# Performance work log

Hardware: AMD Instinct MI355X
Metric: run time of the kernel (lower is better)

The kernel has to match this reference:

```python
import jax, jax.numpy as jnp
import numpy as np

N, T = 64, 256
V, E, K = 32000, 256, 128


def setup_inputs() -> dict:
    key = jax.random.key(0)
    ks = jax.random.split(key, 7)
    x = jax.random.randint(ks[0], (N, T), 0, V)
    embed_w = jax.random.normal(ks[1], (V, E), dtype=jnp.float32) * 0.02
    # nn.Linear(embed_dim, K*K, bias=False), weight.uniform_(-1, 1)
    trans_w = jax.random.uniform(ks[2], (K * K, E), dtype=jnp.float32, minval=-1.0, maxval=1.0)
    # nn.Linear(1, K): weight [K,1], bias [K]
    start_w = jax.random.normal(ks[3], (K, 1), dtype=jnp.float32)
    start_b = jax.random.normal(ks[4], (K,), dtype=jnp.float32) * 0.1
    # nn.Embedding(K, K) cluster embeddings
    emb_cluster_w = jax.random.normal(ks[5], (K, K), dtype=jnp.float32)
    # nn.Linear(K, vocab, bias=False), weight.uniform_(-1, 1) -> weight [V, K]
    emit_w = jax.random.uniform(ks[6], (V, K), dtype=jnp.float32, minval=-1.0, maxval=1.0)
    return {"x": x, "embed_w": embed_w, "trans_w": trans_w, "start_w": start_w,
            "start_b": start_b, "emb_cluster_w": emb_cluster_w, "emit_w": emit_w}


def reference(x, embed_w, trans_w, start_w, start_b, emb_cluster_w, emit_w):
    n, t = x.shape
    k = emb_cluster_w.shape[0]
    ex = embed_w[x]                                            # [N,T,E]
    # Emissions: log_softmax(emit(emb_cluster(i))) per cluster -> [K,V]
    log_emit = jax.nn.log_softmax(emb_cluster_w @ emit_w.T, axis=-1)
    log_emit_t = log_emit.T                                    # [V,K]
    # start(dummy): ones[N,1] @ W.T + b = W[:,0]+b, same per row
    pre = jax.nn.log_softmax(start_w[:, 0] + start_b)          # [K]
    pre = jnp.broadcast_to(pre, (n, k))
    xs = (jnp.swapaxes(ex[:, :-1, :], 0, 1),                   # [T-1,N,E]
          x[:, 1:].T)                                          # [T-1,N]
    def step(pre_alpha, inp):
        x_prev, w_t = inp
        tran = jax.nn.log_softmax((x_prev @ trans_w.T).reshape(n, k, k), axis=-1)
        cur = jax.nn.logsumexp(pre_alpha[:, :, None] + tran, axis=1)   # [N,K]
        cur = cur + log_emit_t[w_t]                            # add log p(w_t | state)
        return cur, None
    cur, _ = jax.lax.scan(step, pre, xs)
    return -jnp.mean(jax.nn.logsumexp(cur, axis=1))
```

## Files before the change

kernel.cpp:

```cpp
#include <hip/hip_runtime.h>
#include <cstdint>
#include <cstddef>

#define N_SEQ 64
#define T_LEN 256
#define VOCAB 32000
#define EDIM  256
#define KS    128
#define KK    16384
#define MROWS 16384
#define MREAL 16320
#define GPART 16

typedef short  short8  __attribute__((ext_vector_type(8)));
typedef float  floatx4 __attribute__((ext_vector_type(4)));
typedef int    intx8   __attribute__((ext_vector_type(8)));

#define LGKM_BARRIER() asm volatile("s_waitcnt lgkmcnt(0)\n\ts_barrier" ::: "memory")
#define LGKM_WAIT()    asm volatile("s_waitcnt lgkmcnt(0)" ::: "memory")

static __device__ __forceinline__ unsigned short f2bf(float f) {
  unsigned u = __float_as_uint(f);
  u += 0x7fffu + ((u >> 16) & 1u);
  return (unsigned short)(u >> 16);
}

static __device__ __forceinline__ float fast_rcp(float x) {
#if __has_builtin(__builtin_amdgcn_rcpf)
  return __builtin_amdgcn_rcpf(x);
#else
  return 1.0f / x;
#endif
}

static __device__ __forceinline__ void gl_lds16(const void* gptr, void* lptr) {
  __builtin_amdgcn_global_load_lds(
      (const __attribute__((address_space(1))) void*)gptr,
      (__attribute__((address_space(3))) void*)lptr, 16, 0, 0);
}

__global__ __launch_bounds__(128) void k_prep(const float* sw, const float* sb, float* pre0) {
  __shared__ float vals[KS];
  __shared__ float MM, LS;
  int tid = threadIdx.x;
  float v = sw[tid] + sb[tid];
  vals[tid] = v;
  __syncthreads();
  if (tid == 0) { float m = vals[0]; for (int i = 1; i < KS; ++i) m = fmaxf(m, vals[i]); MM = m; }
  __syncthreads();
  float e = __expf(v - MM);
  vals[tid] = e;
  __syncthreads();
  if (tid == 0) { float s = 0.f; for (int i = 0; i < KS; ++i) s += vals[i]; LS = MM + __logf(s); }
  __syncthreads();
  pre0[tid] = v - LS;
}

__global__ __launch_bounds__(256) void k_transcvt(const float* tw, unsigned short* tb) {
  int idx = blockIdx.x * 256 + threadIdx.x;
  if (idx >= (KK * EDIM) / 4) return;
  int row = idx >> 6, e4 = idx & 63;
  int rowp = ((row & 127) << 7) | (row >> 7);
  int e4s = (e4 & 0x31) | (((((e4 >> 1) & 7) ^ (rowp & 7))) << 1);
  float4 v = *(const float4*)&tw[(size_t)idx * 4];
  unsigned h0 = f2bf(v.x), h1 = f2bf(v.y), h2 = f2bf(v.z), h3 = f2bf(v.w);
  uint2 o; o.x = h0 | (h1 << 16); o.y = h2 | (h3 << 16);
  *(uint2*)&tb[(size_t)rowp * EDIM + e4s * 4] = o;
}

__global__ __launch_bounds__(256) void k_embed(const int* x, const float* ew, unsigned short* exb) {
  int m = blockIdx.x, e = threadIdx.x;
  int t = m >> 6, n = m & 63;
  float v = 0.f;
  if (m < MREAL) { int tok = x[n * T_LEN + t]; v = ew[(size_t)tok * EDIM + e]; }
  int es = (e & 0xC7) | ((((e >> 3) & 7) ^ (m & 7)) << 3);
  exb[(size_t)m * EDIM + es] = f2bf(v);
}

__global__ __launch_bounds__(256) void k_emitlogits(const float* ecl, const float* emw, float* C) {
  int v0 = blockIdx.x * 64, k0 = blockIdx.y * 64;
  int tid = threadIdx.x;
  __shared__ alignas(16) float At[64 * 17];
  __shared__ alignas(16) float Bt[64 * 17];
  int tx = tid & 15, ty = tid >> 4;
  int r = tid >> 2, q = tid & 3;
  float acc[4][4] = {};
  for (int d0 = 0; d0 < KS; d0 += 16) {
    float4 av = *(const float4*)&ecl[(size_t)(k0 + r) * KS + d0 + q * 4];
    float4 bv = *(const float4*)&emw[(size_t)(v0 + r) * KS + d0 + q * 4];
    __syncthreads();
    At[r * 17 + q * 4 + 0] = av.x; At[r * 17 + q * 4 + 1] = av.y;
    At[r * 17 + q * 4 + 2] = av.z; At[r * 17 + q * 4 + 3] = av.w;
    Bt[r * 17 + q * 4 + 0] = bv.x; Bt[r * 17 + q * 4 + 1] = bv.y;
    Bt[r * 17 + q * 4 + 2] = bv.z; Bt[r * 17 + q * 4 + 3] = bv.w;
    __syncthreads();
    #pragma unroll
    for (int dd = 0; dd < 16; ++dd) {
      float a[4], b[4];
      #pragma unroll
      for (int i = 0; i < 4; ++i) a[i] = At[(ty * 4 + i) * 17 + dd];
      #pragma unroll
      for (int i = 0; i < 4; ++i) b[i] = Bt[(tx * 4 + i) * 17 + dd];
      #pragma unroll
      for (int i = 0; i < 4; ++i)
        #pragma unroll
        for (int jj = 0; jj < 4; ++jj) acc[i][jj] += a[i] * b[jj];
    }
  }
  #pragma unroll
  for (int i = 0; i < 4; ++i) {
    float4 o; o.x = acc[i][0]; o.y = acc[i][1]; o.z = acc[i][2]; o.w = acc[i][3];
    *(float4*)&C[(size_t)(k0 + ty * 4 + i) * VOCAB + v0 + tx * 4] = o;
  }
}

__global__ __launch_bounds__(256) void k_lsec(const float* C, float* lseC) {
  int k = blockIdx.x, tid = threadIdx.x;
  __shared__ float sm[4], ss[4];
  const float* row = C + (size_t)k * VOCAB;
  float m = -1e30f;
  for (int v = tid; v < VOCAB; v += 256) m = fmaxf(m, row[v]);
  #pragma unroll
  for (int s = 1; s < 64; s <<= 1) m = fmaxf(m, __shfl_xor(m, s));
  if ((tid & 63) == 0) sm[tid >> 6] = m;
  __syncthreads();
  m = fmaxf(fmaxf(sm[0], sm[1]), fmaxf(sm[2], sm[3]));
  float sum = 0.f;
  for (int v = tid; v < VOCAB; v += 256) sum += __expf(row[v] - m);
  #pragma unroll
  for (int s = 1; s < 64; s <<= 1) sum += __shfl_xor(sum, s);
  if ((tid & 63) == 0) ss[tid >> 6] = sum;
  __syncthreads();
  if (tid == 0) lseC[k] = m + __logf(ss[0] + ss[1] + ss[2] + ss[3]);
}

__global__ __launch_bounds__(128) void k_emis(const int* x, const float* C, const float* lseC,
                                              float* emis, float* emax) {
  int t = blockIdx.x + 1;
  int n = blockIdx.y;
  int k = threadIdx.x;
  __shared__ float red[2];
  int w = x[n * T_LEN + t];
  float v = C[(size_t)k * VOCAB + w] - lseC[k];
  emis[(size_t)((n << 8) + t) * KS + k] = v;
  float m = v;
  #pragma unroll
  for (int s = 1; s < 64; s <<= 1) m = fmaxf(m, __shfl_xor(m, s));
  if ((k & 63) == 0) red[k >> 6] = m;
  __syncthreads();
  if (k == 0) emax[n * T_LEN + t] = fmaxf(red[0], red[1]);
}

__global__ __launch_bounds__(256) void k_comb(const float* srowP, float* srowR, float* wcomb,
                                              const float* emis, const float* emax,
                                              int m_base, int Rcap, int rows) {
  int id = blockIdx.x * 256 + threadIdx.x;
  if (id >= rows * KS) return;
  float s = 0.f;
  #pragma unroll
  for (int g = 0; g < GPART; ++g) s += srowP[(size_t)g * Rcap * KS + id];
  float r = 1.0f / s;
  srowR[(size_t)m_base * KS + id] = r;
  int m = m_base + (id >> 7);
  int t = m >> 6, n = m & 63, k = id & 127;
  float wv = 0.f;
  if (t >= 1) {
    float e  = emis[(size_t)((n << 8) + t) * KS + k];
    float ex = emax[n * T_LEN + t];
    wv = __expf(e - ex) * r * 4096.0f;
  }
  wcomb[(size_t)m_base * KS + id] = wv;
}

static __device__ __forceinline__ void scan_load_S(const unsigned char* Sbase,
                                                   int l15, int kg, intx8 (&sf)[8]) {
  #pragma unroll
  for (int q = 0; q < 8; ++q) {
    const uint4* p = (const uint4*)(Sbase + (size_t)(q * 16 + l15) * 128 + kg * 32);
    uint4 a = p[0], b = p[1];
    sf[q][0] = a.x; sf[q][1] = a.y; sf[q][2] = a.z; sf[q][3] = a.w;
    sf[q][4] = b.x; sf[q][5] = b.y; sf[q][6] = b.z; sf[q][7] = b.w;
  }
}

static __device__ __forceinline__ void scan_step2(
    int t, int t0, int tLast, int n, int l15, int kg,
    const unsigned char* Sc, const float* wcomb, const float* emax,
    unsigned char* uL8, intx8 (&sf)[8], intx8& uf,
    float (&wv)[8], float& exR, float& M) {
  const float LNS = 8.317766167f;
  floatx4 cz = {0.f, 0.f, 0.f, 0.f};
  float cv[8];
  #pragma unroll
  for (int q = 0; q < 8; ++q) {
    floatx4 d = __builtin_amdgcn_mfma_scale_f32_16x16x128_f8f6f4(
        uf, sf[q], cz, 0, 0, 0, 0x7F7F7F7F, 0, 0x7F7F7F7F);
    cv[q] = d[0];
  }
  int tp = t + 2; if (tp > tLast) tp = tLast;
  scan_load_S(Sc + (size_t)((tp - t0) * 64 + n) * KK, l15, kg, sf);
  float c0 = __uint_as_float(__builtin_amdgcn_readfirstlane(__float_as_uint(cv[0])));
  float rc = fast_rcp(c0);
  #pragma unroll
  for (int q = 0; q < 8; ++q) {
    float up = cv[q] * wv[q] * rc;
    int pk = __builtin_amdgcn_cvt_pk_fp8_f32(up, up, 0, 0);
    uL8[q * 16 + l15] = (unsigned char)(pk & 0xff);
  }
  M += exR + __logf(c0) - LNS;
  #pragma unroll
  for (int q = 0; q < 8; ++q) wv[q] = wcomb[(size_t)(tp * 64 + n) * KS + q * 16 + l15];
  exR = emax[n * T_LEN + tp];
  LGKM_WAIT();
  {
    uint4 ua = *(const uint4*)&uL8[kg * 32];
    uint4 ub = *(const uint4*)&uL8[kg * 32 + 16];
    uf[0] = ua.x; uf[1] = ua.y; uf[2] = ua.z; uf[3] = ua.w;
    uf[4] = ub.x; uf[5] = ub.y; uf[6] = ub.z; uf[7] = ub.w;
  }
}

__global__ __launch_bounds__(256, 2) void k_fused(
    const unsigned short* exb, const unsigned short* trb,
    unsigned char* Sg, float* srowP, int m_base, int Rcap,
    const unsigned char* Ss, const float* srowR, const float* wcomb,
    const float* emis, const float* emax, const float* pre0,
    float* alphaG, float* nll, int t0s, int tcs) {
  __shared__ alignas(16) unsigned short As[128 * 64];
  __shared__ alignas(16) unsigned short Bs[128 * 64];
  __shared__ alignas(16) unsigned char uL8[KS];

  if (blockIdx.x < 64) {
    if (tcs <= 0 || threadIdx.x >= 64) return;
    int n = blockIdx.x;
    int L = threadIdx.x, l15 = L & 15, kg = L >> 4;
    const float SCALE = 4096.0f;
    const float LNS = 8.317766167f;
    int t1 = t0s + tcs, tLast = t1 - 1;
    const float* a0 = (t0s == 1) ? pre0 : (alphaG + (size_t)n * KS);
    float pre[8];
    #pragma unroll
    for (int q = 0; q < 8; ++q) pre[q] = a0[q * 16 + l15];
    float mx = pre[0];
    #pragma unroll
    for (int q = 1; q < 8; ++q) mx = fmaxf(mx, pre[q]);
    #pragma unroll
    for (int s2 = 1; s2 < 16; s2 <<= 1) mx = fmaxf(mx, __shfl_xor(mx, s2));
    float M = mx;
    #pragma unroll
    for (int q = 0; q < 8; ++q) {
      float r0 = srowR[(size_t)((t0s - 1) * 64 + n) * KS + q * 16 + l15];
      float up = __expf(pre[q] - M) * r0 * SCALE;
      int pk = __builtin_amdgcn_cvt_pk_fp8_f32(up, up, 0, 0);
      uL8[q * 16 + l15] = (unsigned char)(pk & 0xff);
    }
    LGKM_WAIT();
    intx8 uf;
    {
      uint4 ua = *(const uint4*)&uL8[kg * 32];
      uint4 ub = *(const uint4*)&uL8[kg * 32 + 16];
      uf[0] = ua.x; uf[1] = ua.y; uf[2] = ua.z; uf[3] = ua.w;
      uf[4] = ub.x; uf[5] = ub.y; uf[6] = ub.z; uf[7] = ub.w;
    }
    intx8 sfA[8], sfB[8];
    scan_load_S(Ss + (size_t)n * KK, l15, kg, sfA);
    int tB = (t0s + 1 < t1) ? (t0s + 1) : tLast;
    scan_load_S(Ss + (size_t)((tB - t0s) * 64 + n) * KK, l15, kg, sfB);
    float wA[8], wB[8];
    #pragma unroll
    for (int q = 0; q < 8; ++q) {
      wA[q] = wcomb[(size_t)(t0s * 64 + n) * KS + q * 16 + l15];
      wB[q] = wcomb[(size_t)(tB * 64 + n) * KS + q * 16 + l15];
    }
    float exA = emax[n * T_LEN + t0s];
    float exB = emax[n * T_LEN + tB];
    int t = t0s;
    while (t < tLast) {
      scan_step2(t, t0s, tLast, n, l15, kg, Ss, wcomb, emax, uL8, sfA, uf, wA, exA, M);
      ++t;
      if (t >= tLast) break;
      scan_step2(t, t0s, tLast, n, l15, kg, Ss, wcomb, emax, uL8, sfB, uf, wB, exB, M);
      ++t;
    }
    {
      floatx4 cz = {0.f, 0.f, 0.f, 0.f};
      float cv[8];
      #pragma unroll
      for (int q = 0; q < 8; ++q) {
        floatx4 d = __builtin_amdgcn_mfma_scale_f32_16x16x128_f8f6f4(
            uf, sfA[q], cz, 0, 0, 0, 0x7F7F7F7F, 0, 0x7F7F7F7F);
        cv[q] = d[0];
      }
      #pragma unroll
      for (int q = 0; q < 8; ++q) {
        float em = emis[(size_t)((n << 8) + tLast) * KS + q * 16 + l15];
        pre[q] = M - LNS + __logf(cv[q]) + em;
      }
    }
    #pragma unroll
    for (int q = 0; q < 8; ++q) alphaG[(size_t)n * KS + q * 16 + l15] = pre[q];
    if (t1 == T_LEN) {
      float m2 = pre[0];
      #pragma unroll
      for (int q = 1; q < 8; ++q) m2 = fmaxf(m2, pre[q]);
      #pragma unroll
      for (int s2 = 1; s2 < 16; s2 <<= 1) m2 = fmaxf(m2, __shfl_xor(m2, s2));
      float e = 0.f;
      #pragma unroll
      for (int q = 0; q < 8; ++q) e += __expf(pre[q] - m2);
      #pragma unroll
      for (int s2 = 1; s2 < 16; s2 <<= 1) e += __shfl_xor(e, s2);
      if (L == 0) nll[n] = m2 + __logf(e);
    }
    return;
  }

  int g = blockIdx.x - 64;
  int bx = g >> 4, grp = g & 15;
  int tid = threadIdx.x, wv = tid >> 6, ln = tid & 63;
  int wc = wv & 1, wm = wv >> 1;
  int m0 = m_base + bx * 128;
  int lr = ln & 15, lk = (ln >> 4) * 8;
  int lg = ln >> 4;
  floatx4 sacc[4][4] = {};
  for (int byi = 0; byi < 8; ++byi) {
    int by = grp * 8 + byi;
    int c0 = by * 128;
    floatx4 acc[4][4] = {};
    for (int k0 = 0; k0 < EDIM; k0 += 64) {
      #pragma unroll
      for (int r = 0; r < 4; ++r) {
        int chunk = (wv * 4 + r) * 64 + ln;
        int row = chunk >> 3, c8 = chunk & 7;
        gl_lds16(&exb[(size_t)(m0 + row) * EDIM + k0 + c8 * 8], &As[(wv * 4 + r) * 512]);
        gl_lds16(&trb[(size_t)(c0 + row) * EDIM + k0 + c8 * 8], &Bs[(wv * 4 + r) * 512]);
      }
      __syncthreads();
      #pragma unroll
      for (int kk = 0; kk < 64; kk += 32) {
        int sw = ((((kk + lk) >> 3) ^ (lr & 7)) << 3);
        short8 af[4], bf[4];
        #pragma unroll
        for (int f = 0; f < 4; ++f)
          af[f] = *(const short8*)&As[(wm * 64 + f * 16 + lr) * 64 + sw];
        #pragma unroll
        for (int f = 0; f < 4; ++f)
          bf[f] = *(const short8*)&Bs[(wc * 64 + f * 16 + lr) * 64 + sw];
        #pragma unroll
        for (int fc = 0; fc < 4; ++fc)
          #pragma unroll
          for (int fm = 0; fm < 4; ++fm)
            acc[fc][fm] = __builtin_amdgcn_mfma_f32_16x16x32_bf16(bf[fc], af[fm], acc[fc][fm], 0, 0, 0);
      }
      LGKM_BARRIER();
    }
    unsigned char* Ts = (unsigned char*)As;
    #pragma unroll
    for (int fc = 0; fc < 4; ++fc) {
      #pragma unroll
      for (int fm = 0; fm < 4; ++fm) {
        floatx4 a = acc[fc][fm];
        float e0 = __expf(a[0]), e1 = __expf(a[1]), e2 = __expf(a[2]), e3 = __expf(a[3]);
        int p = __builtin_amdgcn_cvt_pk_fp8_f32(e0, e1, 0, 0);
        p = __builtin_amdgcn_cvt_pk_fp8_f32(e2, e3, p, 1);
        int mloc = wm * 64 + fm * 16 + lr;
        int cl = wc * 64 + fc * 16 + lg * 4;
        *(int*)&Ts[mloc * 128 + (cl ^ ((mloc & 7) << 4))] = p;
        sacc[fc][fm][0] += e0; sacc[fc][fm][1] += e1;
        sacc[fc][fm][2] += e2; sacc[fc][fm][3] += e3;
      }
    }
    LGKM_BARRIER();
    #pragma unroll
    for (int r = 0; r < 4; ++r) {
      int seg = r * 256 + tid;
      int mloc = seg >> 3, s = seg & 7;
      uint4 v = *(const uint4*)&Ts[mloc * 128 + ((s ^ (mloc & 7)) << 4)];
      *(uint4*)&Sg[(size_t)(bx * 128 + mloc) * KK + c0 + s * 16] = v;
    }
    LGKM_BARRIER();
  }
  #pragma unroll
  for (int fc = 0; fc < 4; ++fc) {
    #pragma unroll
    for (int fm = 0; fm < 4; ++fm) {
      int mloc = bx * 128 + wm * 64 + fm * 16 + lr;
      int i = wc * 64 + fc * 16 + lg * 4;
      *(floatx4*)&srowP[((size_t)grp * Rcap + mloc) * KS + i] = sacc[fc][fm];
    }
  }
}

__global__ __launch_bounds__(64) void k_final(const float* nll, float* out) {
  int tid = threadIdx.x;
  float v = nll[tid];
  #pragma unroll
  for (int s = 1; s < 64; s <<= 1) v += __shfl_xor(v, s);
  if (tid == 0) out[0] = -v / 64.0f;
}

extern "C" void kernel_launch(void* const* d_in, const int* in_sizes, int n_in,
                              void* d_out, int out_size, void* d_ws, size_t ws_size,
                              hipStream_t stream) {
  const int*   x       = (const int*)d_in[0];
  const float* embed_w = (const float*)d_in[1];
  const float* trans_w = (const float*)d_in[2];
  const float* start_w = (const float*)d_in[3];
  const float* start_b = (const float*)d_in[4];
  const float* ecl     = (const float*)d_in[5];
  const float* emw     = (const float*)d_in[6];

  char* w = (char*)d_ws;
  size_t off = 0;
  auto alloc = [&](size_t bytes) -> char* {
    char* p = w + off;
    off = (off + bytes + 255) & ~(size_t)255;
    return p;
  };
  float*          pre0   = (float*)alloc(KS * 4);
  float*          lseC   = (float*)alloc(KS * 4);
  float*          nll    = (float*)alloc(N_SEQ * 4);
  float*          alphaG = (float*)alloc((size_t)N_SEQ * KS * 4);
  float*          emax   = (float*)alloc((size_t)N_SEQ * T_LEN * 4);
  unsigned short* trb    = (unsigned short*)alloc((size_t)KK * EDIM * 2);
  unsigned short* exb    = (unsigned short*)alloc((size_t)MROWS * EDIM * 2);
  float*          emis   = (float*)alloc((size_t)N_SEQ * T_LEN * KS * 4);
  float*          srowR  = (float*)alloc((size_t)MROWS * KS * 4);
  float*          wcomb  = (float*)alloc((size_t)MROWS * KS * 4);
  char* region = w + off;
  size_t avail = (ws_size > off) ? (ws_size - off) : 0;
  float* C = (float*)region;

  int Tc = 2;
  for (int c = 2; c <= 64; c += 2)
    if ((size_t)c * 64 * 40960 <= avail) Tc = c;
  int Rcap = Tc * 64;
  unsigned char* S0    = (unsigned char*)region;
  unsigned char* S1    = (unsigned char*)(region + (size_t)Rcap * KK);
  float*         srowP = (float*)(region + (size_t)2 * Rcap * KK);

  hipLaunchKernelGGL(k_prep,       dim3(1),        dim3(128), 0, stream, start_w, start_b, pre0);
  hipLaunchKernelGGL(k_transcvt,   dim3(4096),     dim3(256), 0, stream, trans_w, trb);
  hipLaunchKernelGGL(k_embed,      dim3(16384),    dim3(256), 0, stream, x, embed_w, exb);
  hipLaunchKernelGGL(k_emitlogits, dim3(500, 2),   dim3(256), 0, stream, ecl, emw, C);
  hipLaunchKernelGGL(k_lsec,       dim3(128),      dim3(256), 0, stream, C, lseC);
  hipLaunchKernelGGL(k_emis,       dim3(255, 64),  dim3(128), 0, stream, x, C, lseC, emis, emax);

  int ct0[140], ctc[140], nc = 0;
  {
    int t0 = 1;
    while (t0 < T_LEN) {
      int tc = T_LEN - t0; if (tc > Tc) tc = Tc;
      ct0[nc] = t0; ctc[nc] = tc; ++nc; t0 += tc;
    }
  }
  for (int c = 0; c <= nc; ++c) {
    bool hasG = (c < nc), hasS = (c > 0);
    int gx = 0, m_base = 0;
    if (hasG) { gx = (ctc[c] * 64 + 127) / 128; m_base = (ct0[c] - 1) * 64; }
    unsigned char* Sg = (c & 1) ? S1 : S0;
    unsigned char* Ssc = ((c - 1) & 1) ? S1 : S0;
    int t0s = hasS ? ct0[c - 1] : 0;
    int tcs = hasS ? ctc[c - 1] : 0;
    hipLaunchKernelGGL(k_fused, dim3(64 + gx * 16), dim3(256), 0, stream,
                       exb, trb, Sg, srowP, m_base, Rcap,
                       Ssc, srowR, wcomb, emis, emax, pre0, alphaG, nll, t0s, tcs);
    if (hasG)
      hipLaunchKernelGGL(k_comb, dim3(gx * 64), dim3(256), 0, stream,
                         srowP, srowR, wcomb, emis, emax, m_base, Rcap, gx * 128);
  }
  hipLaunchKernelGGL(k_final, dim3(1), dim3(64), 0, stream, nll, (float*)d_out);
}
```

Measured before the change: 576.3 us.

## Stage scan transition tiles into LDS with triple-buffered async global-to-LDS loads

The scan blocks now stream each step's fp8 transition tile and combined weights into a three-slot LDS ring using global_load_lds, prefetching two steps ahead and waiting with vmcnt, instead of holding two register copies of the tile. The weight buffer is transposed to an [n,t,k] layout so each step's weights form one contiguous 512-byte load. The per-step emax accumulation is replaced by a single wave reduction at the start, and the logs are summed and applied once at the end. This is meant to hide global latency on the serial recurrence and cut register pressure, at the cost of LDS reads per step and a shared-memory union with the GEMM path.

```diff
diff --git a/kernel.cpp b/kernel.cpp
--- a/kernel.cpp
+++ b/kernel.cpp
@@ -37,6 +37,16 @@
   __builtin_amdgcn_global_load_lds(
       (const __attribute__((address_space(1))) void*)gptr,
       (__attribute__((address_space(3))) void*)lptr, 16, 0, 0);
+}
+
+static __device__ __forceinline__ void stage_S(const unsigned char* src,
+                                               unsigned char* dst, int p) {
+  #pragma unroll
+  for (int j = 0; j < 16; ++j) {
+    int A = j * 1024 + p * 16;
+    int gg = A ^ (((A >> 7) & 7) << 4);
+    gl_lds16(src + gg, dst + j * 1024);
+  }
 }
 
 __global__ __launch_bounds__(128) void k_prep(const float* sw, const float* sb, float* pre0) {
@@ -151,7 +161,7 @@
   if (k == 0) emax[n * T_LEN + t] = fmaxf(red[0], red[1]);
 }
 
-__global__ __launch_bounds__(256) void k_comb(const float* srowP, float* srowR, float* wcomb,
+__global__ __launch_bounds__(256) void k_comb(const float* srowP, float* srowR, float* wcombT,
                                               const float* emis, const float* emax,
                                               int m_base, int Rcap, int rows) {
   int id = blockIdx.x * 256 + threadIdx.x;
@@ -169,73 +179,30 @@
     float ex = emax[n * T_LEN + t];
     wv = __expf(e - ex) * r * 4096.0f;
   }
-  wcomb[(size_t)m_base * KS + id] = wv;
-}
-
-static __device__ __forceinline__ void scan_load_S(const unsigned char* Sbase,
-                                                   int l15, int kg, intx8 (&sf)[8]) {
-  #pragma unroll
-  for (int q = 0; q < 8; ++q) {
-    const uint4* p = (const uint4*)(Sbase + (size_t)(q * 16 + l15) * 128 + kg * 32);
-    uint4 a = p[0], b = p[1];
-    sf[q][0] = a.x; sf[q][1] = a.y; sf[q][2] = a.z; sf[q][3] = a.w;
-    sf[q][4] = b.x; sf[q][5] = b.y; sf[q][6] = b.z; sf[q][7] = b.w;
-  }
-}
-
-static __device__ __forceinline__ void scan_step2(
-    int t, int t0, int tLast, int n, int l15, int kg,
-    const unsigned char* Sc, const float* wcomb, const float* emax,
-    unsigned char* uL8, intx8 (&sf)[8], intx8& uf,
-    float (&wv)[8], float& exR, float& M) {
-  const float LNS = 8.317766167f;
-  floatx4 cz = {0.f, 0.f, 0.f, 0.f};
-  float cv[8];
-  #pragma unroll
-  for (int q = 0; q < 8; ++q) {
-    floatx4 d = __builtin_amdgcn_mfma_scale_f32_16x16x128_f8f6f4(
-        uf, sf[q], cz, 0, 0, 0, 0x7F7F7F7F, 0, 0x7F7F7F7F);
-    cv[q] = d[0];
-  }
-  int tp = t + 2; if (tp > tLast) tp = tLast;
-  scan_load_S(Sc + (size_t)((tp - t0) * 64 + n) * KK, l15, kg, sf);
-  float c0 = __uint_as_float(__builtin_amdgcn_readfirstlane(__float_as_uint(cv[0])));
-  float rc = fast_rcp(c0);
-  #pragma unroll
-  for (int q = 0; q < 8; ++q) {
-    float up = cv[q] * wv[q] * rc;
-    int pk = __builtin_amdgcn_cvt_pk_fp8_f32(up, up, 0, 0);
-    uL8[q * 16 + l15] = (unsigned char)(pk & 0xff);
-  }
-  M += exR + __logf(c0) - LNS;
-  #pragma unroll
-  for (int q = 0; q < 8; ++q) wv[q] = wcomb[(size_t)(tp * 64 + n) * KS + q * 16 + l15];
-  exR = emax[n * T_LEN + tp];
-  LGKM_WAIT();
-  {
-    uint4 ua = *(const uint4*)&uL8[kg * 32];
-    uint4 ub = *(const uint4*)&uL8[kg * 32 + 16];
-    uf[0] = ua.x; uf[1] = ua.y; uf[2] = ua.z; uf[3] = ua.w;
-    uf[4] = ub.x; uf[5] = ub.y; uf[6] = ub.z; uf[7] = ub.w;
-  }
+  wcombT[((size_t)n * T_LEN + t) * KS + k] = wv;
 }
 
 __global__ __launch_bounds__(256, 2) void k_fused(
     const unsigned short* exb, const unsigned short* trb,
     unsigned char* Sg, float* srowP, int m_base, int Rcap,
-    const unsigned char* Ss, const float* srowR, const float* wcomb,
+    const unsigned char* Ss, const float* srowR, const float* wcombT,
     const float* emis, const float* emax, const float* pre0,
     float* alphaG, float* nll, int t0s, int tcs) {
-  __shared__ alignas(16) unsigned short As[128 * 64];
-  __shared__ alignas(16) unsigned short Bs[128 * 64];
+  __shared__ union alignas(16) {
+    struct { unsigned short As[128 * 64]; unsigned short Bs[128 * 64]; } g;
+    struct { unsigned char S3[3][16384]; unsigned char aux3[3][1024]; } s;
+  } sh;
   __shared__ alignas(16) unsigned char uL8[KS];
 
   if (blockIdx.x < 64) {
     if (tcs <= 0 || threadIdx.x >= 64) return;
     int n = blockIdx.x;
-    int L = threadIdx.x, l15 = L & 15, kg = L >> 4;
+    int p = threadIdx.x;
+    int l15 = p & 15, kg = p >> 4;
+    int swz = (l15 & 7) << 4;
     const float SCALE = 4096.0f;
     const float LNS = 8.317766167f;
+    int L = tcs;
     int t1 = t0s + tcs, tLast = t1 - 1;
     const float* a0 = (t0s == 1) ? pre0 : (alphaG + (size_t)n * KS);
     float pre[8];
@@ -247,6 +214,10 @@
     #pragma unroll
     for (int s2 = 1; s2 < 16; s2 <<= 1) mx = fmaxf(mx, __shfl_xor(mx, s2));
     float M = mx;
+    float ev = (p < L - 1) ? emax[n * T_LEN + t0s + p] : 0.f;
+    #pragma unroll
+    for (int s2 = 1; s2 < 64; s2 <<= 1) ev += __shfl_xor(ev, s2);
+    float exSum = ev;
     #pragma unroll
     for (int q = 0; q < 8; ++q) {
       float r0 = srowR[(size_t)((t0s - 1) * 64 + n) * KS + q * 16 + l15];
@@ -255,6 +226,7 @@
       uL8[q * 16 + l15] = (unsigned char)(pk & 0xff);
     }
     LGKM_WAIT();
+    __builtin_amdgcn_sched_barrier(0);
     intx8 uf;
     {
       uint4 ua = *(const uint4*)&uL8[kg * 32];
@@ -262,40 +234,63 @@
       uf[0] = ua.x; uf[1] = ua.y; uf[2] = ua.z; uf[3] = ua.w;
       uf[4] = ub.x; uf[5] = ub.y; uf[6] = ub.z; uf[7] = ub.w;
     }
-    intx8 sfA[8], sfB[8];
-    scan_load_S(Ss + (size_t)n * KK, l15, kg, sfA);
-    int tB = (t0s + 1 < t1) ? (t0s + 1) : tLast;
-    scan_load_S(Ss + (size_t)((tB - t0s) * 64 + n) * KK, l15, kg, sfB);
-    float wA[8], wB[8];
-    #pragma unroll
-    for (int q = 0; q < 8; ++q) {
-      wA[q] = wcomb[(size_t)(t0s * 64 + n) * KS + q * 16 + l15];
-      wB[q] = wcomb[(size_t)(tB * 64 + n) * KS + q * 16 + l15];
-    }
-    float exA = emax[n * T_LEN + t0s];
-    float exB = emax[n * T_LEN + tB];
-    int t = t0s;
-    while (t < tLast) {
-      scan_step2(t, t0s, tLast, n, l15, kg, Ss, wcomb, emax, uL8, sfA, uf, wA, exA, M);
-      ++t;
-      if (t >= tLast) break;
-      scan_step2(t, t0s, tLast, n, l15, kg, Ss, wcomb, emax, uL8, sfB, uf, wB, exB, M);
-      ++t;
-    }
-    {
+    const unsigned char* wcb = (const unsigned char*)wcombT;
+    stage_S(Ss + (size_t)n * KK, &sh.s.S3[0][0], p);
+    gl_lds16(wcb + ((size_t)n * T_LEN + t0s) * 512 + (size_t)p * 16, &sh.s.aux3[0][0]);
+    int i1 = (1 < L) ? 1 : (L - 1);
+    stage_S(Ss + (size_t)(i1 * 64 + n) * KK, &sh.s.S3[1][0], p);
+    gl_lds16(wcb + ((size_t)n * T_LEN + (t0s + i1)) * 512 + (size_t)p * 16, &sh.s.aux3[1][0]);
+
+    float logSum = 0.f;
+    int bu = 0, bs = 2;
+    for (int i = 0; i < L; ++i) {
+      int ip2 = i + 2; if (ip2 > L - 1) ip2 = L - 1;
+      stage_S(Ss + (size_t)(ip2 * 64 + n) * KK, &sh.s.S3[bs][0], p);
+      gl_lds16(wcb + ((size_t)n * T_LEN + (t0s + ip2)) * 512 + (size_t)p * 16, &sh.s.aux3[bs][0]);
+      asm volatile("s_waitcnt vmcnt(34)" ::: "memory");
+      __builtin_amdgcn_sched_barrier(0);
+      const unsigned char* Sb = &sh.s.S3[bu][0];
       floatx4 cz = {0.f, 0.f, 0.f, 0.f};
       float cv[8];
       #pragma unroll
       for (int q = 0; q < 8; ++q) {
+        int ab = (((q * 16 + l15) * 128) + kg * 32) ^ swz;
+        uint4 aa = *(const uint4*)&Sb[ab];
+        uint4 bb = *(const uint4*)&Sb[ab ^ 16];
+        intx8 sf;
+        sf[0] = aa.x; sf[1] = aa.y; sf[2] = aa.z; sf[3] = aa.w;
+        sf[4] = bb.x; sf[5] = bb.y; sf[6] = bb.z; sf[7] = bb.w;
         floatx4 d = __builtin_amdgcn_mfma_scale_f32_16x16x128_f8f6f4(
-            uf, sfA[q], cz, 0, 0, 0, 0x7F7F7F7F, 0, 0x7F7F7F7F);
+            uf, sf, cz, 0, 0, 0, 0x7F7F7F7F, 0, 0x7F7F7F7F);
         cv[q] = d[0];
       }
-      #pragma unroll
-      for (int q = 0; q < 8; ++q) {
-        float em = emis[(size_t)((n << 8) + tLast) * KS + q * 16 + l15];
-        pre[q] = M - LNS + __logf(cv[q]) + em;
+      if (i < L - 1) {
+        float c0 = __uint_as_float(__builtin_amdgcn_readfirstlane(__float_as_uint(cv[0])));
+        float rc = fast_rcp(c0);
+        const float* wvp = (const float*)&sh.s.aux3[bu][0];
+        #pragma unroll
+        for (int q = 0; q < 8; ++q) {
+          float up = cv[q] * wvp[q * 16 + l15] * rc;
+          int pk = __builtin_amdgcn_cvt_pk_fp8_f32(up, up, 0, 0);
+          uL8[q * 16 + l15] = (unsigned char)(pk & 0xff);
+        }
+        logSum += __logf(c0);
+        LGKM_WAIT();
+        __builtin_amdgcn_sched_barrier(0);
+        uint4 ua = *(const uint4*)&uL8[kg * 32];
+        uint4 ub = *(const uint4*)&uL8[kg * 32 + 16];
+        uf[0] = ua.x; uf[1] = ua.y; uf[2] = ua.z; uf[3] = ua.w;
+        uf[4] = ub.x; uf[5] = ub.y; uf[6] = ub.z; uf[7] = ub.w;
+      } else {
+        float Mf = M + exSum + logSum - (float)(L - 1) * LNS;
+        #pragma unroll
+        for (int q = 0; q < 8; ++q) {
+          float em = emis[(size_t)((n << 8) + tLast) * KS + q * 16 + l15];
+          pre[q] = Mf - LNS + __logf(cv[q]) + em;
+        }
       }
+      bu = (bu == 2) ? 0 : bu + 1;
+      bs = (bs == 2) ? 0 : bs + 1;
     }
     #pragma unroll
     for (int q = 0; q < 8; ++q) alphaG[(size_t)n * KS + q * 16 + l15] = pre[q];
@@ -310,7 +305,7 @@
       for (int q = 0; q < 8; ++q) e += __expf(pre[q] - m2);
       #pragma unroll
       for (int s2 = 1; s2 < 16; s2 <<= 1) e += __shfl_xor(e, s2);
-      if (L == 0) nll[n] = m2 + __logf(e);
+      if (p == 0) nll[n] = m2 + __logf(e);
     }
     return;
   }
@@ -332,8 +327,8 @@
       for (int r = 0; r < 4; ++r) {
         int chunk = (wv * 4 + r) * 64 + ln;
         int row = chunk >> 3, c8 = chunk & 7;
-        gl_lds16(&exb[(size_t)(m0 + row) * EDIM + k0 + c8 * 8], &As[(wv * 4 + r) * 512]);
-        gl_lds16(&trb[(size_t)(c0 + row) * EDIM + k0 + c8 * 8], &Bs[(wv * 4 + r) * 512]);
+        gl_lds16(&exb[(size_t)(m0 + row) * EDIM + k0 + c8 * 8], &sh.g.As[(wv * 4 + r) * 512]);
+        gl_lds16(&trb[(size_t)(c0 + row) * EDIM + k0 + c8 * 8], &sh.g.Bs[(wv * 4 + r) * 512]);
       }
       __syncthreads();
       #pragma unroll
@@ -342,10 +337,10 @@
         short8 af[4], bf[4];
         #pragma unroll
         for (int f = 0; f < 4; ++f)
-          af[f] = *(const short8*)&As[(wm * 64 + f * 16 + lr) * 64 + sw];
+          af[f] = *(const short8*)&sh.g.As[(wm * 64 + f * 16 + lr) * 64 + sw];
         #pragma unroll
         for (int f = 0; f < 4; ++f)
-          bf[f] = *(const short8*)&Bs[(wc * 64 + f * 16 + lr) * 64 + sw];
+          bf[f] = *(const short8*)&sh.g.Bs[(wc * 64 + f * 16 + lr) * 64 + sw];
         #pragma unroll
         for (int fc = 0; fc < 4; ++fc)
           #pragma unroll
@@ -354,18 +349,18 @@
       }
       LGKM_BARRIER();
     }
-    unsigned char* Ts = (unsigned char*)As;
+    unsigned char* Ts = (unsigned char*)sh.g.As;
     #pragma unroll
     for (int fc = 0; fc < 4; ++fc) {
       #pragma unroll
       for (int fm = 0; fm < 4; ++fm) {
         floatx4 a = acc[fc][fm];
         float e0 = __expf(a[0]), e1 = __expf(a[1]), e2 = __expf(a[2]), e3 = __expf(a[3]);
-        int p = __builtin_amdgcn_cvt_pk_fp8_f32(e0, e1, 0, 0);
-        p = __builtin_amdgcn_cvt_pk_fp8_f32(e2, e3, p, 1);
+        int pq = __builtin_amdgcn_cvt_pk_fp8_f32(e0, e1, 0, 0);
+        pq = __builtin_amdgcn_cvt_pk_fp8_f32(e2, e3, pq, 1);
         int mloc = wm * 64 + fm * 16 + lr;
         int cl = wc * 64 + fc * 16 + lg * 4;
-        *(int*)&Ts[mloc * 128 + (cl ^ ((mloc & 7) << 4))] = p;
+        *(int*)&Ts[mloc * 128 + (cl ^ ((mloc & 7) << 4))] = pq;
         sacc[fc][fm][0] += e0; sacc[fc][fm][1] += e1;
         sacc[fc][fm][2] += e2; sacc[fc][fm][3] += e3;
       }
@@ -426,7 +421,7 @@
   unsigned short* exb    = (unsigned short*)alloc((size_t)MROWS * EDIM * 2);
   float*          emis   = (float*)alloc((size_t)N_SEQ * T_LEN * KS * 4);
   float*          srowR  = (float*)alloc((size_t)MROWS * KS * 4);
-  float*          wcomb  = (float*)alloc((size_t)MROWS * KS * 4);
+  float*          wcombT = (float*)alloc((size_t)N_SEQ * T_LEN * KS * 4);
   char* region = w + off;
   size_t avail = (ws_size > off) ? (ws_size - off) : 0;
   float* C = (float*)region;
@@ -464,10 +459,10 @@
     int tcs = hasS ? ctc[c - 1] : 0;
     hipLaunchKernelGGL(k_fused, dim3(64 + gx * 16), dim3(256), 0, stream,
                        exb, trb, Sg, srowP, m_base, Rcap,
-                       Ssc, srowR, wcomb, emis, emax, pre0, alphaG, nll, t0s, tcs);
+                       Ssc, srowR, wcombT, emis, emax, pre0, alphaG, nll, t0s, tcs);
     if (hasG)
       hipLaunchKernelGGL(k_comb, dim3(gx * 64), dim3(256), 0, stream,
-                         srowP, srowR, wcomb, emis, emax, m_base, Rcap, gx * 128);
+                         srowP, srowR, wcombT, emis, emax, m_base, Rcap, gx * 128);
   }
   hipLaunchKernelGGL(k_final, dim3(1), dim3(64), 0, stream, nll, (float*)d_out);
 }
```

Result: slower. 612.3 us (+6.2%).

## Replace partial-sum buffers and combine kernel with atomic row-sum accumulation

Applied to the files above, without the earlier changes.

The GEMM blocks now atomically add their per-group row sums directly into a zeroed srowS buffer, instead of writing 16 partial slices that a separate k_comb kernel reduced into reciprocals and combined emission weights. The scan now computes the emission weights on the fly from emis, emax and srowS, with emax values held in one register per lane and fetched by shuffle. The final step is folded into the step loop. This removes one kernel launch per chunk and a large intermediate buffer, which frees workspace for bigger chunks. In exchange it adds contention from many float atomics and a little extra exp/rcp work on the serial scan path.

```diff
diff --git a/kernel.cpp b/kernel.cpp
--- a/kernel.cpp
+++ b/kernel.cpp
@@ -10,7 +10,6 @@
 #define KK    16384
 #define MROWS 16384
 #define MREAL 16320
-#define GPART 16
 
 typedef short  short8  __attribute__((ext_vector_type(8)));
 typedef float  floatx4 __attribute__((ext_vector_type(4)));
@@ -37,6 +36,12 @@
   __builtin_amdgcn_global_load_lds(
       (const __attribute__((address_space(1))) void*)gptr,
       (__attribute__((address_space(3))) void*)lptr, 16, 0, 0);
+}
+
+__global__ __launch_bounds__(256) void k_zero(float* p) {
+  size_t i = (size_t)blockIdx.x * 256 + threadIdx.x;
+  floatx4 z = {0.f, 0.f, 0.f, 0.f};
+  *(floatx4*)&p[i * 4] = z;
 }
 
 __global__ __launch_bounds__(128) void k_prep(const float* sw, const float* sb, float* pre0) {
@@ -151,27 +156,6 @@
   if (k == 0) emax[n * T_LEN + t] = fmaxf(red[0], red[1]);
 }
 
-__global__ __launch_bounds__(256) void k_comb(const float* srowP, float* srowR, float* wcomb,
-                                              const float* emis, const float* emax,
-                                              int m_base, int Rcap, int rows) {
-  int id = blockIdx.x * 256 + threadIdx.x;
-  if (id >= rows * KS) return;
-  float s = 0.f;
-  #pragma unroll
-  for (int g = 0; g < GPART; ++g) s += srowP[(size_t)g * Rcap * KS + id];
-  float r = 1.0f / s;
-  srowR[(size_t)m_base * KS + id] = r;
-  int m = m_base + (id >> 7);
-  int t = m >> 6, n = m & 63, k = id & 127;
-  float wv = 0.f;
-  if (t >= 1) {
-    float e  = emis[(size_t)((n << 8) + t) * KS + k];
-    float ex = emax[n * T_LEN + t];
-    wv = __expf(e - ex) * r * 4096.0f;
-  }
-  wcomb[(size_t)m_base * KS + id] = wv;
-}
-
 static __device__ __forceinline__ void scan_load_S(const unsigned char* Sbase,
                                                    int l15, int kg, intx8 (&sf)[8]) {
   #pragma unroll
@@ -183,11 +167,11 @@
   }
 }
 
-static __device__ __forceinline__ void scan_step2(
-    int t, int t0, int tLast, int n, int l15, int kg,
-    const unsigned char* Sc, const float* wcomb, const float* emax,
+static __device__ __forceinline__ void scan_step3(
+    int t, int t0, int tLast, int n, int l15, int kg, bool last,
+    const unsigned char* Sc, const float* emis, const float* srowS, float ev,
     unsigned char* uL8, intx8 (&sf)[8], intx8& uf,
-    float (&wv)[8], float& exR, float& M) {
+    float (&wv)[8], float& M, float (&pre)[8]) {
   const float LNS = 8.317766167f;
   floatx4 cz = {0.f, 0.f, 0.f, 0.f};
   float cv[8];
@@ -199,33 +183,43 @@
   }
   int tp = t + 2; if (tp > tLast) tp = tLast;
   scan_load_S(Sc + (size_t)((tp - t0) * 64 + n) * KK, l15, kg, sf);
-  float c0 = __uint_as_float(__builtin_amdgcn_readfirstlane(__float_as_uint(cv[0])));
-  float rc = fast_rcp(c0);
-  #pragma unroll
-  for (int q = 0; q < 8; ++q) {
-    float up = cv[q] * wv[q] * rc;
-    int pk = __builtin_amdgcn_cvt_pk_fp8_f32(up, up, 0, 0);
-    uL8[q * 16 + l15] = (unsigned char)(pk & 0xff);
-  }
-  M += exR + __logf(c0) - LNS;
-  #pragma unroll
-  for (int q = 0; q < 8; ++q) wv[q] = wcomb[(size_t)(tp * 64 + n) * KS + q * 16 + l15];
-  exR = emax[n * T_LEN + tp];
-  LGKM_WAIT();
-  {
+  if (!last) {
+    float c0 = __uint_as_float(__builtin_amdgcn_readfirstlane(__float_as_uint(cv[0])));
+    float rc = fast_rcp(c0);
+    #pragma unroll
+    for (int q = 0; q < 8; ++q) {
+      float up = cv[q] * wv[q] * rc;
+      int pk = __builtin_amdgcn_cvt_pk_fp8_f32(up, up, 0, 0);
+      uL8[q * 16 + l15] = (unsigned char)(pk & 0xff);
+    }
+    float exI = __shfl(ev, t - t0);
+    M += exI + __logf(c0) - LNS;
+    float ex2 = __shfl(ev, tp - t0);
+    #pragma unroll
+    for (int q = 0; q < 8; ++q) {
+      float em = emis[(size_t)((n << 8) + tp) * KS + q * 16 + l15];
+      float sq = srowS[(size_t)(tp * 64 + n) * KS + q * 16 + l15];
+      wv[q] = __expf(em - ex2) * 4096.0f * fast_rcp(sq);
+    }
+    LGKM_WAIT();
     uint4 ua = *(const uint4*)&uL8[kg * 32];
     uint4 ub = *(const uint4*)&uL8[kg * 32 + 16];
     uf[0] = ua.x; uf[1] = ua.y; uf[2] = ua.z; uf[3] = ua.w;
     uf[4] = ub.x; uf[5] = ub.y; uf[6] = ub.z; uf[7] = ub.w;
+  } else {
+    #pragma unroll
+    for (int q = 0; q < 8; ++q) {
+      float em = emis[(size_t)((n << 8) + tLast) * KS + q * 16 + l15];
+      pre[q] = M - LNS + __logf(cv[q]) + em;
+    }
   }
 }
 
 __global__ __launch_bounds__(256, 2) void k_fused(
     const unsigned short* exb, const unsigned short* trb,
-    unsigned char* Sg, float* srowP, int m_base, int Rcap,
-    const unsigned char* Ss, const float* srowR, const float* wcomb,
-    const float* emis, const float* emax, const float* pre0,
-    float* alphaG, float* nll, int t0s, int tcs) {
+    unsigned char* Sg, float* srowS, int m_base,
+    const unsigned char* Ss, const float* emis, const float* emax,
+    const float* pre0, float* alphaG, float* nll, int t0s, int tcs) {
   __shared__ alignas(16) unsigned short As[128 * 64];
   __shared__ alignas(16) unsigned short Bs[128 * 64];
   __shared__ alignas(16) unsigned char uL8[KS];
@@ -233,9 +227,9 @@
   if (blockIdx.x < 64) {
     if (tcs <= 0 || threadIdx.x >= 64) return;
     int n = blockIdx.x;
-    int L = threadIdx.x, l15 = L & 15, kg = L >> 4;
+    int p = threadIdx.x, l15 = p & 15, kg = p >> 4;
     const float SCALE = 4096.0f;
-    const float LNS = 8.317766167f;
+    int L = tcs;
     int t1 = t0s + tcs, tLast = t1 - 1;
     const float* a0 = (t0s == 1) ? pre0 : (alphaG + (size_t)n * KS);
     float pre[8];
@@ -247,10 +241,11 @@
     #pragma unroll
     for (int s2 = 1; s2 < 16; s2 <<= 1) mx = fmaxf(mx, __shfl_xor(mx, s2));
     float M = mx;
+    float ev = (p < L) ? emax[n * T_LEN + t0s + p] : 0.f;
     #pragma unroll
     for (int q = 0; q < 8; ++q) {
-      float r0 = srowR[(size_t)((t0s - 1) * 64 + n) * KS + q * 16 + l15];
-      float up = __expf(pre[q] - M) * r0 * SCALE;
+      float s0 = srowS[(size_t)((t0s - 1) * 64 + n) * KS + q * 16 + l15];
+      float up = __expf(pre[q] - M) * SCALE * fast_rcp(s0);
       int pk = __builtin_amdgcn_cvt_pk_fp8_f32(up, up, 0, 0);
       uL8[q * 16 + l15] = (unsigned char)(pk & 0xff);
     }
@@ -264,38 +259,32 @@
     }
     intx8 sfA[8], sfB[8];
     scan_load_S(Ss + (size_t)n * KK, l15, kg, sfA);
-    int tB = (t0s + 1 < t1) ? (t0s + 1) : tLast;
-    scan_load_S(Ss + (size_t)((tB - t0s) * 64 + n) * KK, l15, kg, sfB);
+    int tB0 = (t0s + 1 < t1) ? (t0s + 1) : tLast;
+    scan_load_S(Ss + (size_t)((tB0 - t0s) * 64 + n) * KK, l15, kg, sfB);
     float wA[8], wB[8];
-    #pragma unroll
-    for (int q = 0; q < 8; ++q) {
-      wA[q] = wcomb[(size_t)(t0s * 64 + n) * KS + q * 16 + l15];
-      wB[q] = wcomb[(size_t)(tB * 64 + n) * KS + q * 16 + l15];
-    }
-    float exA = emax[n * T_LEN + t0s];
-    float exB = emax[n * T_LEN + tB];
+    {
+      float exA = __shfl(ev, 0);
+      float exB = __shfl(ev, tB0 - t0s);
+      #pragma unroll
+      for (int q = 0; q < 8; ++q) {
+        float emA = emis[(size_t)((n << 8) + t0s) * KS + q * 16 + l15];
+        float sA  = srowS[(size_t)(t0s * 64 + n) * KS + q * 16 + l15];
+        wA[q] = __expf(emA - exA) * SCALE * fast_rcp(sA);
+        float emB = emis[(size_t)((n << 8) + tB0) * KS + q * 16 + l15];
+        float sB  = srowS[(size_t)(tB0 * 64 + n) * KS + q * 16 + l15];
+        wB[q] = __expf(emB - exB) * SCALE * fast_rcp(sB);
+      }
+    }
     int t = t0s;
-    while (t < tLast) {
-      scan_step2(t, t0s, tLast, n, l15, kg, Ss, wcomb, emax, uL8, sfA, uf, wA, exA, M);
+    for (;;) {
+      scan_step3(t, t0s, tLast, n, l15, kg, (t == tLast), Ss, emis, srowS, ev,
+                 uL8, sfA, uf, wA, M, pre);
+      if (t == tLast) break;
       ++t;
-      if (t >= tLast) break;
-      scan_step2(t, t0s, tLast, n, l15, kg, Ss, wcomb, emax, uL8, sfB, uf, wB, exB, M);
+      scan_step3(t, t0s, tLast, n, l15, kg, (t == tLast), Ss, emis, srowS, ev,
+                 uL8, sfB, uf, wB, M, pre);
+      if (t == tLast) break;
       ++t;
-    }
-    {
-      floatx4 cz = {0.f, 0.f, 0.f, 0.f};
-      float cv[8];
-      #pragma unroll
-      for (int q = 0; q < 8; ++q) {
-        floatx4 d = __builtin_amdgcn_mfma_scale_f32_16x16x128_f8f6f4(
-            uf, sfA[q], cz, 0, 0, 0, 0x7F7F7F7F, 0, 0x7F7F7F7F);
-        cv[q] = d[0];
-      }
-      #pragma unroll
-      for (int q = 0; q < 8; ++q) {
-        float em = emis[(size_t)((n << 8) + tLast) * KS + q * 16 + l15];
-        pre[q] = M - LNS + __logf(cv[q]) + em;
-      }
     }
     #pragma unroll
     for (int q = 0; q < 8; ++q) alphaG[(size_t)n * KS + q * 16 + l15] = pre[q];
@@ -310,7 +299,7 @@
       for (int q = 0; q < 8; ++q) e += __expf(pre[q] - m2);
       #pragma unroll
       for (int s2 = 1; s2 < 16; s2 <<= 1) e += __shfl_xor(e, s2);
-      if (L == 0) nll[n] = m2 + __logf(e);
+      if (p == 0) nll[n] = m2 + __logf(e);
     }
     return;
   }
@@ -361,11 +350,11 @@
       for (int fm = 0; fm < 4; ++fm) {
         floatx4 a = acc[fc][fm];
         float e0 = __expf(a[0]), e1 = __expf(a[1]), e2 = __expf(a[2]), e3 = __expf(a[3]);
-        int p = __builtin_amdgcn_cvt_pk_fp8_f32(e0, e1, 0, 0);
-        p = __builtin_amdgcn_cvt_pk_fp8_f32(e2, e3, p, 1);
+        int pq = __builtin_amdgcn_cvt_pk_fp8_f32(e0, e1, 0, 0);
+        pq = __builtin_amdgcn_cvt_pk_fp8_f32(e2, e3, pq, 1);
         int mloc = wm * 64 + fm * 16 + lr;
         int cl = wc * 64 + fc * 16 + lg * 4;
-        *(int*)&Ts[mloc * 128 + (cl ^ ((mloc & 7) << 4))] = p;
+        *(int*)&Ts[mloc * 128 + (cl ^ ((mloc & 7) << 4))] = pq;
         sacc[fc][fm][0] += e0; sacc[fc][fm][1] += e1;
         sacc[fc][fm][2] += e2; sacc[fc][fm][3] += e3;
       }
@@ -385,8 +374,12 @@
     #pragma unroll
     for (int fm = 0; fm < 4; ++fm) {
       int mloc = bx * 128 + wm * 64 + fm * 16 + lr;
-      int i = wc * 64 + fc * 16 + lg * 4;
-      *(floatx4*)&srowP[((size_t)grp * Rcap + mloc) * KS + i] = sacc[fc][fm];
+      int ii = wc * 64 + fc * 16 + lg * 4;
+      float* dp = &srowS[(size_t)(m_base + mloc) * KS + ii];
+      atomicAdd(dp + 0, sacc[fc][fm][0]);
+      atomicAdd(dp + 1, sacc[fc][fm][1]);
+      atomicAdd(dp + 2, sacc[fc][fm][2]);
+      atomicAdd(dp + 3, sacc[fc][fm][3]);
     }
   }
 }
@@ -425,20 +418,19 @@
   unsigned short* trb    = (unsigned short*)alloc((size_t)KK * EDIM * 2);
   unsigned short* exb    = (unsigned short*)alloc((size_t)MROWS * EDIM * 2);
   float*          emis   = (float*)alloc((size_t)N_SEQ * T_LEN * KS * 4);
-  float*          srowR  = (float*)alloc((size_t)MROWS * KS * 4);
-  float*          wcomb  = (float*)alloc((size_t)MROWS * KS * 4);
+  float*          srowS  = (float*)alloc((size_t)MROWS * KS * 4);
   char* region = w + off;
   size_t avail = (ws_size > off) ? (ws_size - off) : 0;
   float* C = (float*)region;
 
   int Tc = 2;
   for (int c = 2; c <= 64; c += 2)
-    if ((size_t)c * 64 * 40960 <= avail) Tc = c;
+    if ((size_t)c * 64 * 32768 <= avail) Tc = c;
   int Rcap = Tc * 64;
-  unsigned char* S0    = (unsigned char*)region;
-  unsigned char* S1    = (unsigned char*)(region + (size_t)Rcap * KK);
-  float*         srowP = (float*)(region + (size_t)2 * Rcap * KK);
-
+  unsigned char* S0 = (unsigned char*)region;
+  unsigned char* S1 = (unsigned char*)(region + (size_t)Rcap * KK);
+
+  hipLaunchKernelGGL(k_zero,       dim3(MROWS * KS / 1024), dim3(256), 0, stream, srowS);
   hipLaunchKernelGGL(k_prep,       dim3(1),        dim3(128), 0, stream, start_w, start_b, pre0);
   hipLaunchKernelGGL(k_transcvt,   dim3(4096),     dim3(256), 0, stream, trans_w, trb);
   hipLaunchKernelGGL(k_embed,      dim3(16384),    dim3(256), 0, stream, x, embed_w, exb);
@@ -463,11 +455,8 @@
     int t0s = hasS ? ct0[c - 1] : 0;
     int tcs = hasS ? ctc[c - 1] : 0;
     hipLaunchKernelGGL(k_fused, dim3(64 + gx * 16), dim3(256), 0, stream,
-                       exb, trb, Sg, srowP, m_base, Rcap,
-                       Ssc, srowR, wcomb, emis, emax, pre0, alphaG, nll, t0s, tcs);
-    if (hasG)
-      hipLaunchKernelGGL(k_comb, dim3(gx * 64), dim3(256), 0, stream,
-                         srowP, srowR, wcomb, emis, emax, m_base, Rcap, gx * 128);
+                       exb, trb, Sg, srowS, m_base,
+                       Ssc, emis, emax, pre0, alphaG, nll, t0s, tcs);
   }
   hipLaunchKernelGGL(k_final, dim3(1), dim3(64), 0, stream, nll, (float*)d_out);
 }
```

Result: slower. 928.9 us (+61.2%).
